# Optimization experiments

Measured on AMD Instinct MI355X. Metric: run time of the kernel, lower is better.

## Reference

```python
import jax, jax.numpy as jnp
import numpy as np

SQ, B, H, D = 2048, 1, 16, 64
HIDDEN = H * D


def setup_inputs() -> dict:
    key = jax.random.key(0)
    kq, kk, kv = jax.random.split(key, 3)
    query_layer = jax.random.normal(kq, (SQ, B, H, D), dtype=jnp.float32)
    key_layer = jax.random.normal(kk, (SQ, B, H, D), dtype=jnp.float32)
    value_layer = jax.random.normal(kv, (SQ, B, H, D), dtype=jnp.float32)
    return {"query_layer": query_layer, "key_layer": key_layer, "value_layer": value_layer}


def reference(query_layer, key_layer, value_layer):
    sq, b, h, d = query_layer.shape
    sk = key_layer.shape[0]
    norm = 1.0 / jnp.sqrt(jnp.asarray(d, dtype=query_layer.dtype))
    # scores: [b, h, sq, sk]  (materialized in the original via baddbmm)
    scores = jnp.einsum('sbhd,tbhd->bhst', query_layer, key_layer) * norm
    # causal mask (tril over [sq, sk]); masked positions -> -10000.0 as in original
    causal = jnp.tril(jnp.ones((sq, sk), dtype=bool))
    scores = jnp.where(causal[None, None], scores, jnp.asarray(-10000.0, scores.dtype))
    probs = jax.nn.softmax(scores, axis=-1)
    # context: [sq, b, h, d] -> [sq, b, hidden]
    ctx = jnp.einsum('bhst,tbhd->sbhd', probs, value_layer)
    return ctx.reshape(sq, b, h * d)
```

## Files before the change

kernel.cpp:

```cpp
#include <hip/hip_runtime.h>

typedef __bf16 bf16_t;
typedef bf16_t bf16x4 __attribute__((ext_vector_type(4)));
typedef bf16_t bf16x8 __attribute__((ext_vector_type(8)));
typedef float f32x4 __attribute__((ext_vector_type(4)));
typedef float f32x16 __attribute__((ext_vector_type(16)));

namespace {
constexpr int kNH  = 16;
constexpr int kHD  = 64;
constexpr int kHID = kNH * kHD;
constexpr int kSQ  = 2048;
constexpr int kKP  = 72;
constexpr int kOmPitch = 68;
constexpr int kSmBytes = 71680;
constexpr int kKbElems = kNH * kSQ * kHD;
}

__global__ __launch_bounds__(256)
void prep_kernel(const float* __restrict__ Kg, const float* __restrict__ Vg,
                 bf16_t* __restrict__ Kb, bf16_t* __restrict__ Vb) {
  const int bid = blockIdx.x;
  const int tid = threadIdx.x;
  if (bid < 1024) {
    const int o    = (bid * 256 + tid) * 8;
    const int head = o >> 17;
    const int t    = (o >> 6) & 2047;
    const int d0   = o & 63;
    const float4 f0 = *(const float4*)(Kg + (size_t)t * kHID + head * kHD + d0);
    const float4 f1 = *(const float4*)(Kg + (size_t)t * kHID + head * kHD + d0 + 4);
    bf16x8 hk;
    hk[0] = (bf16_t)f0.x; hk[1] = (bf16_t)f0.y; hk[2] = (bf16_t)f0.z; hk[3] = (bf16_t)f0.w;
    hk[4] = (bf16_t)f1.x; hk[5] = (bf16_t)f1.y; hk[6] = (bf16_t)f1.z; hk[7] = (bf16_t)f1.w;
    *(bf16x8*)(Kb + o) = hk;
  } else {
    const int vb   = bid - 1024;
    const int head = vb >> 6;
    const int tile = vb & 63;
    const int lane = tid >> 2;
    const int hh   = lane >> 5;
    const int m31  = lane & 31;
    const int q    = tid & 3;
    const int db   = q >> 1, tp = q & 1;
    const int tb   = tile * 32 + 4 * hh + 16 * tp;
    const int d    = m31 + 32 * db;
    const float* src = Vg + (size_t)tb * kHID + head * kHD + d;
    bf16x8 hv;
    #pragma unroll
    for (int j = 0; j < 8; ++j)
      hv[j] = (bf16_t)src[(size_t)((j & 3) + 8 * (j >> 2)) * kHID];
    *(bf16x8*)(Vb + ((size_t)(head * 64 + tile) * 64 + lane) * 32 + (db * 16 + tp * 8)) = hv;
  }
}

__global__ __launch_bounds__(512, 2)
void fattn_kernel(const float* __restrict__ Qg, const bf16_t* __restrict__ Kb,
                  const bf16_t* __restrict__ Vb, float* __restrict__ Og) {
  __shared__ __align__(16) unsigned char smraw[kSmBytes];
  bf16_t* sm = (bf16_t*)smraw;
  bf16_t* qs = sm;

  const int bid  = blockIdx.x;
  const int head = bid & (kNH - 1);
  const int ip   = bid >> 4;

  const int tid  = threadIdx.x;
  const int wave = tid >> 6;
  const int lane = tid & 63;
  const int h    = lane >> 5;
  const int m31  = lane & 31;

  const float kQScale = 0.125f * 1.44269504088896340736f;

  const bf16_t* kfb = Kb + (size_t)head * (kSQ * kHD) + (size_t)m31 * kHD + 8 * h;
  const bf16_t* vfb = Vb + ((size_t)head * 64 * 64 + lane) * 32;

  for (int halfq = 0; halfq < 2; ++halfq) {
    const int mblk = halfq ? ip : (31 - ip);
    const int m0   = mblk * 64;
    const int mtk  = 2 * mblk + 1;

    __syncthreads();
    #pragma unroll
    for (int i = 0; i < 2; ++i) {
      const int idx = tid + 512 * i;
      const int row = idx >> 4;
      const int c4  = (idx & 15) * 4;
      const float4 f = *(const float4*)(Qg + (size_t)(m0 + row) * kHID + head * kHD + c4);
      bf16x4 qv;
      qv[0] = (bf16_t)(f.x * kQScale); qv[1] = (bf16_t)(f.y * kQScale);
      qv[2] = (bf16_t)(f.z * kQScale); qv[3] = (bf16_t)(f.w * kQScale);
      *(bf16x4*)(qs + row * kKP + c4) = qv;
    }
    __syncthreads();

    bf16x8 qf00 = *(const bf16x8*)(qs + m31 * kKP +  0 + 8 * h);
    bf16x8 qf01 = *(const bf16x8*)(qs + m31 * kKP + 16 + 8 * h);
    bf16x8 qf02 = *(const bf16x8*)(qs + m31 * kKP + 32 + 8 * h);
    bf16x8 qf03 = *(const bf16x8*)(qs + m31 * kKP + 48 + 8 * h);
    bf16x8 qf10 = *(const bf16x8*)(qs + (32 + m31) * kKP +  0 + 8 * h);
    bf16x8 qf11 = *(const bf16x8*)(qs + (32 + m31) * kKP + 16 + 8 * h);
    bf16x8 qf12 = *(const bf16x8*)(qs + (32 + m31) * kKP + 32 + 8 * h);
    bf16x8 qf13 = *(const bf16x8*)(qs + (32 + m31) * kKP + 48 + 8 * h);

    f32x16 Oa00, Oa10, Oa01, Oa11;
    #pragma unroll
    for (int r = 0; r < 16; ++r) { Oa00[r] = 0.f; Oa10[r] = 0.f; Oa01[r] = 0.f; Oa11[r] = 0.f; }
    float lacc0 = 0.f, lacc1 = 0.f;

    bf16x8 k0, k1, k2, k3, v0, v1, v2, v3;
    int jt = wave;
    if (jt <= mtk) {
      const bf16_t* kp = kfb + (size_t)jt * 2048;
      k0 = *(const bf16x8*)(kp);      k1 = *(const bf16x8*)(kp + 16);
      k2 = *(const bf16x8*)(kp + 32); k3 = *(const bf16x8*)(kp + 48);
      const bf16_t* vp = vfb + (size_t)jt * 2048;
      v0 = *(const bf16x8*)(vp);      v1 = *(const bf16x8*)(vp + 8);
      v2 = *(const bf16x8*)(vp + 16); v3 = *(const bf16x8*)(vp + 24);
    }
    for (; jt <= mtk; jt += 8) {
      const int kv0  = jt * 32;
      const bool do0 = (kv0 <= m0);

      f32x16 c0, c1;
      if (do0) {
        #pragma unroll
        for (int r = 0; r < 16; ++r) c0[r] = 0.f;
        c0 = __builtin_amdgcn_mfma_f32_32x32x16_bf16(k0, qf00, c0, 0, 0, 0);
        c0 = __builtin_amdgcn_mfma_f32_32x32x16_bf16(k1, qf01, c0, 0, 0, 0);
        c0 = __builtin_amdgcn_mfma_f32_32x32x16_bf16(k2, qf02, c0, 0, 0, 0);
        c0 = __builtin_amdgcn_mfma_f32_32x32x16_bf16(k3, qf03, c0, 0, 0, 0);
      }
      #pragma unroll
      for (int r = 0; r < 16; ++r) c1[r] = 0.f;
      c1 = __builtin_amdgcn_mfma_f32_32x32x16_bf16(k0, qf10, c1, 0, 0, 0);
      c1 = __builtin_amdgcn_mfma_f32_32x32x16_bf16(k1, qf11, c1, 0, 0, 0);
      c1 = __builtin_amdgcn_mfma_f32_32x32x16_bf16(k2, qf12, c1, 0, 0, 0);
      c1 = __builtin_amdgcn_mfma_f32_32x32x16_bf16(k3, qf13, c1, 0, 0, 0);

      if (jt + 8 <= mtk) {
        const bf16_t* kp = kfb + (size_t)(jt + 8) * 2048;
        k0 = *(const bf16x8*)(kp);      k1 = *(const bf16x8*)(kp + 16);
        k2 = *(const bf16x8*)(kp + 32); k3 = *(const bf16x8*)(kp + 48);
      }

      if (do0) {
        float p[16];
        if (kv0 == m0) {
          #pragma unroll
          for (int r = 0; r < 16; ++r) {
            const int kr = (r & 3) + 8 * (r >> 2) + 4 * h;
            const float e = __builtin_amdgcn_exp2f(c0[r]);
            p[r] = (kr <= m31) ? e : 0.f;
            lacc0 += p[r];
          }
        } else {
          #pragma unroll
          for (int r = 0; r < 16; ++r) { p[r] = __builtin_amdgcn_exp2f(c0[r]); lacc0 += p[r]; }
        }
        bf16x8 pb0, pb1;
        #pragma unroll
        for (int j = 0; j < 8; ++j) { pb0[j] = (bf16_t)p[j]; pb1[j] = (bf16_t)p[8 + j]; }
        Oa00 = __builtin_amdgcn_mfma_f32_32x32x16_bf16(v0, pb0, Oa00, 0, 0, 0);
        Oa10 = __builtin_amdgcn_mfma_f32_32x32x16_bf16(v2, pb0, Oa10, 0, 0, 0);
        Oa00 = __builtin_amdgcn_mfma_f32_32x32x16_bf16(v1, pb1, Oa00, 0, 0, 0);
        Oa10 = __builtin_amdgcn_mfma_f32_32x32x16_bf16(v3, pb1, Oa10, 0, 0, 0);
      }

      {
        float p[16];
        if (kv0 == m0 + 32) {
          #pragma unroll
          for (int r = 0; r < 16; ++r) {
            const int kr = (r & 3) + 8 * (r >> 2) + 4 * h;
            const float e = __builtin_amdgcn_exp2f(c1[r]);
            p[r] = (kr <= m31) ? e : 0.f;
            lacc1 += p[r];
          }
        } else {
          #pragma unroll
          for (int r = 0; r < 16; ++r) { p[r] = __builtin_amdgcn_exp2f(c1[r]); lacc1 += p[r]; }
        }
        bf16x8 pb0, pb1;
        #pragma unroll
        for (int j = 0; j < 8; ++j) { pb0[j] = (bf16_t)p[j]; pb1[j] = (bf16_t)p[8 + j]; }
        Oa01 = __builtin_amdgcn_mfma_f32_32x32x16_bf16(v0, pb0, Oa01, 0, 0, 0);
        Oa11 = __builtin_amdgcn_mfma_f32_32x32x16_bf16(v2, pb0, Oa11, 0, 0, 0);
        Oa01 = __builtin_amdgcn_mfma_f32_32x32x16_bf16(v1, pb1, Oa01, 0, 0, 0);
        Oa11 = __builtin_amdgcn_mfma_f32_32x32x16_bf16(v3, pb1, Oa11, 0, 0, 0);
      }

      if (jt + 8 <= mtk) {
        const bf16_t* vp = vfb + (size_t)(jt + 8) * 2048;
        v0 = *(const bf16x8*)(vp);      v1 = *(const bf16x8*)(vp + 8);
        v2 = *(const bf16x8*)(vp + 16); v3 = *(const bf16x8*)(vp + 24);
      }
    }

    float* fv   = (float*)smraw;
    float* Om   = fv + wave * 32 * kOmPitch;
    float* larr = fv + 8 * 32 * kOmPitch;

    #pragma unroll
    for (int qh = 0; qh < 2; ++qh) {
      __syncthreads();
      {
        const f32x16& A0 = qh ? Oa01 : Oa00;
        const f32x16& A1 = qh ? Oa11 : Oa10;
        #pragma unroll
        for (int q = 0; q < 4; ++q) {
          f32x4 w0, w1;
          #pragma unroll
          for (int e = 0; e < 4; ++e) { w0[e] = A0[4 * q + e]; w1[e] = A1[4 * q + e]; }
          *(f32x4*)(Om + (size_t)m31 * kOmPitch + 8 * q + 4 * h)      = w0;
          *(f32x4*)(Om + (size_t)m31 * kOmPitch + 32 + 8 * q + 4 * h) = w1;
        }
        larr[wave * 64 + lane] = qh ? lacc1 : lacc0;
      }
      __syncthreads();
      {
        const int row = tid >> 4;
        const int c4  = (tid & 15) * 4;
        float l = 0.f;
        #pragma unroll
        for (int w = 0; w < 8; ++w)
          l += larr[w * 64 + row] + larr[w * 64 + 32 + row];
        const float inv = 1.f / l;
        f32x4 o;
        #pragma unroll
        for (int e = 0; e < 4; ++e) o[e] = 0.f;
        #pragma unroll
        for (int w = 0; w < 8; ++w) {
          const f32x4 a = *(const f32x4*)(fv + w * 32 * kOmPitch + (size_t)row * kOmPitch + c4);
          #pragma unroll
          for (int e = 0; e < 4; ++e) o[e] += a[e];
        }
        #pragma unroll
        for (int e = 0; e < 4; ++e) o[e] *= inv;
        *(f32x4*)(Og + (size_t)(m0 + 32 * qh + row) * kHID + head * kHD + c4) = o;
      }
    }
  }
}

extern "C" void kernel_launch(void* const* d_in, const int* in_sizes, int n_in,
                              void* d_out, int out_size, void* d_ws, size_t ws_size,
                              hipStream_t stream) {
  (void)in_sizes; (void)n_in; (void)ws_size; (void)out_size;
  const float* Q = (const float*)d_in[0];
  const float* K = (const float*)d_in[1];
  const float* V = (const float*)d_in[2];
  float* O = (float*)d_out;
  bf16_t* Kb = (bf16_t*)d_ws;
  bf16_t* Vb = Kb + kKbElems;
  hipLaunchKernelGGL(prep_kernel, dim3(2048), dim3(256), 0, stream, K, V, Kb, Vb);
  dim3 grid(256);
  dim3 block(512);
  hipLaunchKernelGGL(fattn_kernel, grid, block, 0, stream, Q, Kb, Vb, O);
}
```

Before: 93.04 us.

## Split query tile across wave halves with six KV-group waves each

Blocks grow from 8 to 12 waves. Each wave now computes a single 32-row query tile: waves are split into two halves by query rows, and within a half six waves stride over the KV tiles. This replaces the old scheme where every wave handled both 32-row query halves and wasted MFMA slots on masked tiles, and it puts more waves per CU to hide latency. MFMA sections are wrapped in s_setprio to favour matrix issue, and the epilogue reduces over six partial results per half with one fewer barrier. The cost is more shared memory per block, so fewer blocks can share a CU, and fewer registers per thread.

Result: slower. 102.0 us (+9.6%).

```diff
diff --git a/kernel.cpp b/kernel.cpp
--- a/kernel.cpp
+++ b/kernel.cpp
@@ -13,7 +13,8 @@
 constexpr int kSQ  = 2048;
 constexpr int kKP  = 72;
 constexpr int kOmPitch = 68;
-constexpr int kSmBytes = 71680;
+constexpr int kQBytes  = 9216;
+constexpr int kSmBytes = kQBytes + 12 * 32 * kOmPitch * 4 + 12 * 64 * 4;
 constexpr int kKbElems = kNH * kSQ * kHD;
 }
 
@@ -53,12 +54,11 @@
   }
 }
 
-__global__ __launch_bounds__(512, 2)
+__global__ __launch_bounds__(768, 3)
 void fattn_kernel(const float* __restrict__ Qg, const bf16_t* __restrict__ Kb,
                   const bf16_t* __restrict__ Vb, float* __restrict__ Og) {
   __shared__ __align__(16) unsigned char smraw[kSmBytes];
-  bf16_t* sm = (bf16_t*)smraw;
-  bf16_t* qs = sm;
+  bf16_t* qs = (bf16_t*)smraw;
 
   const int bid  = blockIdx.x;
   const int head = bid & (kNH - 1);
@@ -69,175 +69,148 @@
   const int lane = tid & 63;
   const int h    = lane >> 5;
   const int m31  = lane & 31;
+  const int hw   = wave / 6;
+  const int kg   = wave - 6 * hw;
 
   const float kQScale = 0.125f * 1.44269504088896340736f;
 
   const bf16_t* kfb = Kb + (size_t)head * (kSQ * kHD) + (size_t)m31 * kHD + 8 * h;
   const bf16_t* vfb = Vb + ((size_t)head * 64 * 64 + lane) * 32;
+
+  float* fv   = (float*)(smraw + kQBytes);
+  float* Om   = fv + wave * 32 * kOmPitch;
+  float* larr = fv + 12 * 32 * kOmPitch;
 
   for (int halfq = 0; halfq < 2; ++halfq) {
     const int mblk = halfq ? ip : (31 - ip);
     const int m0   = mblk * 64;
-    const int mtk  = 2 * mblk + 1;
+    const int q0   = m0 + 32 * hw;
+    const int jtmax = 2 * mblk + hw;
 
     __syncthreads();
     #pragma unroll
     for (int i = 0; i < 2; ++i) {
-      const int idx = tid + 512 * i;
-      const int row = idx >> 4;
-      const int c4  = (idx & 15) * 4;
-      const float4 f = *(const float4*)(Qg + (size_t)(m0 + row) * kHID + head * kHD + c4);
-      bf16x4 qv;
-      qv[0] = (bf16_t)(f.x * kQScale); qv[1] = (bf16_t)(f.y * kQScale);
-      qv[2] = (bf16_t)(f.z * kQScale); qv[3] = (bf16_t)(f.w * kQScale);
-      *(bf16x4*)(qs + row * kKP + c4) = qv;
+      const int idx = tid + 768 * i;
+      if (idx < 1024) {
+        const int row = idx >> 4;
+        const int c4  = (idx & 15) * 4;
+        const float4 f = *(const float4*)(Qg + (size_t)(m0 + row) * kHID + head * kHD + c4);
+        bf16x4 qv;
+        qv[0] = (bf16_t)(f.x * kQScale); qv[1] = (bf16_t)(f.y * kQScale);
+        qv[2] = (bf16_t)(f.z * kQScale); qv[3] = (bf16_t)(f.w * kQScale);
+        *(bf16x4*)(qs + row * kKP + c4) = qv;
+      }
     }
     __syncthreads();
 
-    bf16x8 qf00 = *(const bf16x8*)(qs + m31 * kKP +  0 + 8 * h);
-    bf16x8 qf01 = *(const bf16x8*)(qs + m31 * kKP + 16 + 8 * h);
-    bf16x8 qf02 = *(const bf16x8*)(qs + m31 * kKP + 32 + 8 * h);
-    bf16x8 qf03 = *(const bf16x8*)(qs + m31 * kKP + 48 + 8 * h);
-    bf16x8 qf10 = *(const bf16x8*)(qs + (32 + m31) * kKP +  0 + 8 * h);
-    bf16x8 qf11 = *(const bf16x8*)(qs + (32 + m31) * kKP + 16 + 8 * h);
-    bf16x8 qf12 = *(const bf16x8*)(qs + (32 + m31) * kKP + 32 + 8 * h);
-    bf16x8 qf13 = *(const bf16x8*)(qs + (32 + m31) * kKP + 48 + 8 * h);
-
-    f32x16 Oa00, Oa10, Oa01, Oa11;
-    #pragma unroll
-    for (int r = 0; r < 16; ++r) { Oa00[r] = 0.f; Oa10[r] = 0.f; Oa01[r] = 0.f; Oa11[r] = 0.f; }
-    float lacc0 = 0.f, lacc1 = 0.f;
+    const bf16_t* qrow = qs + (32 * hw + m31) * kKP + 8 * h;
+    bf16x8 qf0 = *(const bf16x8*)(qrow +  0);
+    bf16x8 qf1 = *(const bf16x8*)(qrow + 16);
+    bf16x8 qf2 = *(const bf16x8*)(qrow + 32);
+    bf16x8 qf3 = *(const bf16x8*)(qrow + 48);
+
+    f32x16 Oa0, Oa1;
+    #pragma unroll
+    for (int r = 0; r < 16; ++r) { Oa0[r] = 0.f; Oa1[r] = 0.f; }
+    float lacc = 0.f;
 
     bf16x8 k0, k1, k2, k3, v0, v1, v2, v3;
-    int jt = wave;
-    if (jt <= mtk) {
-      const bf16_t* kp = kfb + (size_t)jt * 2048;
+    {
+      const bf16_t* kp = kfb + (size_t)kg * 2048;
       k0 = *(const bf16x8*)(kp);      k1 = *(const bf16x8*)(kp + 16);
       k2 = *(const bf16x8*)(kp + 32); k3 = *(const bf16x8*)(kp + 48);
-      const bf16_t* vp = vfb + (size_t)jt * 2048;
+      const bf16_t* vp = vfb + (size_t)kg * 2048;
       v0 = *(const bf16x8*)(vp);      v1 = *(const bf16x8*)(vp + 8);
       v2 = *(const bf16x8*)(vp + 16); v3 = *(const bf16x8*)(vp + 24);
     }
-    for (; jt <= mtk; jt += 8) {
-      const int kv0  = jt * 32;
-      const bool do0 = (kv0 <= m0);
-
-      f32x16 c0, c1;
-      if (do0) {
-        #pragma unroll
-        for (int r = 0; r < 16; ++r) c0[r] = 0.f;
-        c0 = __builtin_amdgcn_mfma_f32_32x32x16_bf16(k0, qf00, c0, 0, 0, 0);
-        c0 = __builtin_amdgcn_mfma_f32_32x32x16_bf16(k1, qf01, c0, 0, 0, 0);
-        c0 = __builtin_amdgcn_mfma_f32_32x32x16_bf16(k2, qf02, c0, 0, 0, 0);
-        c0 = __builtin_amdgcn_mfma_f32_32x32x16_bf16(k3, qf03, c0, 0, 0, 0);
-      }
+
+    for (int jt = kg; jt <= jtmax; jt += 6) {
+      const int kv0 = jt * 32;
+      const int jn = (jt + 6 <= jtmax) ? (jt + 6) : kg;
+
+      f32x16 c;
       #pragma unroll
-      for (int r = 0; r < 16; ++r) c1[r] = 0.f;
-      c1 = __builtin_amdgcn_mfma_f32_32x32x16_bf16(k0, qf10, c1, 0, 0, 0);
-      c1 = __builtin_amdgcn_mfma_f32_32x32x16_bf16(k1, qf11, c1, 0, 0, 0);
-      c1 = __builtin_amdgcn_mfma_f32_32x32x16_bf16(k2, qf12, c1, 0, 0, 0);
-      c1 = __builtin_amdgcn_mfma_f32_32x32x16_bf16(k3, qf13, c1, 0, 0, 0);
-
-      if (jt + 8 <= mtk) {
-        const bf16_t* kp = kfb + (size_t)(jt + 8) * 2048;
+      for (int r = 0; r < 16; ++r) c[r] = 0.f;
+      __builtin_amdgcn_s_setprio(1);
+      c = __builtin_amdgcn_mfma_f32_32x32x16_bf16(k0, qf0, c, 0, 0, 0);
+      c = __builtin_amdgcn_mfma_f32_32x32x16_bf16(k1, qf1, c, 0, 0, 0);
+      c = __builtin_amdgcn_mfma_f32_32x32x16_bf16(k2, qf2, c, 0, 0, 0);
+      c = __builtin_amdgcn_mfma_f32_32x32x16_bf16(k3, qf3, c, 0, 0, 0);
+      __builtin_amdgcn_s_setprio(0);
+
+      {
+        const bf16_t* kp = kfb + (size_t)jn * 2048;
         k0 = *(const bf16x8*)(kp);      k1 = *(const bf16x8*)(kp + 16);
         k2 = *(const bf16x8*)(kp + 32); k3 = *(const bf16x8*)(kp + 48);
       }
 
-      if (do0) {
-        float p[16];
-        if (kv0 == m0) {
-          #pragma unroll
-          for (int r = 0; r < 16; ++r) {
-            const int kr = (r & 3) + 8 * (r >> 2) + 4 * h;
-            const float e = __builtin_amdgcn_exp2f(c0[r]);
-            p[r] = (kr <= m31) ? e : 0.f;
-            lacc0 += p[r];
-          }
-        } else {
-          #pragma unroll
-          for (int r = 0; r < 16; ++r) { p[r] = __builtin_amdgcn_exp2f(c0[r]); lacc0 += p[r]; }
+      float p[16];
+      if (kv0 == q0) {
+        #pragma unroll
+        for (int r = 0; r < 16; ++r) {
+          const int kr = (r & 3) + 8 * (r >> 2) + 4 * h;
+          const float e = __builtin_amdgcn_exp2f(c[r]);
+          p[r] = (kr <= m31) ? e : 0.f;
+          lacc += p[r];
         }
-        bf16x8 pb0, pb1;
-        #pragma unroll
-        for (int j = 0; j < 8; ++j) { pb0[j] = (bf16_t)p[j]; pb1[j] = (bf16_t)p[8 + j]; }
-        Oa00 = __builtin_amdgcn_mfma_f32_32x32x16_bf16(v0, pb0, Oa00, 0, 0, 0);
-        Oa10 = __builtin_amdgcn_mfma_f32_32x32x16_bf16(v2, pb0, Oa10, 0, 0, 0);
-        Oa00 = __builtin_amdgcn_mfma_f32_32x32x16_bf16(v1, pb1, Oa00, 0, 0, 0);
-        Oa10 = __builtin_amdgcn_mfma_f32_32x32x16_bf16(v3, pb1, Oa10, 0, 0, 0);
-      }
+      } else {
+        #pragma unroll
+        for (int r = 0; r < 16; ++r) { p[r] = __builtin_amdgcn_exp2f(c[r]); lacc += p[r]; }
+      }
+      bf16x8 pb0, pb1;
+      #pragma unroll
+      for (int j = 0; j < 8; ++j) { pb0[j] = (bf16_t)p[j]; pb1[j] = (bf16_t)p[8 + j]; }
+
+      __builtin_amdgcn_s_setprio(1);
+      Oa0 = __builtin_amdgcn_mfma_f32_32x32x16_bf16(v0, pb0, Oa0, 0, 0, 0);
+      Oa1 = __builtin_amdgcn_mfma_f32_32x32x16_bf16(v2, pb0, Oa1, 0, 0, 0);
+      Oa0 = __builtin_amdgcn_mfma_f32_32x32x16_bf16(v1, pb1, Oa0, 0, 0, 0);
+      Oa1 = __builtin_amdgcn_mfma_f32_32x32x16_bf16(v3, pb1, Oa1, 0, 0, 0);
+      __builtin_amdgcn_s_setprio(0);
 
       {
-        float p[16];
-        if (kv0 == m0 + 32) {
-          #pragma unroll
-          for (int r = 0; r < 16; ++r) {
-            const int kr = (r & 3) + 8 * (r >> 2) + 4 * h;
-            const float e = __builtin_amdgcn_exp2f(c1[r]);
-            p[r] = (kr <= m31) ? e : 0.f;
-            lacc1 += p[r];
-          }
-        } else {
-          #pragma unroll
-          for (int r = 0; r < 16; ++r) { p[r] = __builtin_amdgcn_exp2f(c1[r]); lacc1 += p[r]; }
-        }
-        bf16x8 pb0, pb1;
-        #pragma unroll
-        for (int j = 0; j < 8; ++j) { pb0[j] = (bf16_t)p[j]; pb1[j] = (bf16_t)p[8 + j]; }
-        Oa01 = __builtin_amdgcn_mfma_f32_32x32x16_bf16(v0, pb0, Oa01, 0, 0, 0);
-        Oa11 = __builtin_amdgcn_mfma_f32_32x32x16_bf16(v2, pb0, Oa11, 0, 0, 0);
-        Oa01 = __builtin_amdgcn_mfma_f32_32x32x16_bf16(v1, pb1, Oa01, 0, 0, 0);
-        Oa11 = __builtin_amdgcn_mfma_f32_32x32x16_bf16(v3, pb1, Oa11, 0, 0, 0);
-      }
-
-      if (jt + 8 <= mtk) {
-        const bf16_t* vp = vfb + (size_t)(jt + 8) * 2048;
+        const bf16_t* vp = vfb + (size_t)jn * 2048;
         v0 = *(const bf16x8*)(vp);      v1 = *(const bf16x8*)(vp + 8);
         v2 = *(const bf16x8*)(vp + 16); v3 = *(const bf16x8*)(vp + 24);
       }
     }
 
-    float* fv   = (float*)smraw;
-    float* Om   = fv + wave * 32 * kOmPitch;
-    float* larr = fv + 8 * 32 * kOmPitch;
-
-    #pragma unroll
-    for (int qh = 0; qh < 2; ++qh) {
-      __syncthreads();
-      {
-        const f32x16& A0 = qh ? Oa01 : Oa00;
-        const f32x16& A1 = qh ? Oa11 : Oa10;
-        #pragma unroll
-        for (int q = 0; q < 4; ++q) {
-          f32x4 w0, w1;
-          #pragma unroll
-          for (int e = 0; e < 4; ++e) { w0[e] = A0[4 * q + e]; w1[e] = A1[4 * q + e]; }
-          *(f32x4*)(Om + (size_t)m31 * kOmPitch + 8 * q + 4 * h)      = w0;
-          *(f32x4*)(Om + (size_t)m31 * kOmPitch + 32 + 8 * q + 4 * h) = w1;
-        }
-        larr[wave * 64 + lane] = qh ? lacc1 : lacc0;
-      }
-      __syncthreads();
-      {
-        const int row = tid >> 4;
-        const int c4  = (tid & 15) * 4;
+    #pragma unroll
+    for (int q = 0; q < 4; ++q) {
+      f32x4 w0, w1;
+      #pragma unroll
+      for (int e = 0; e < 4; ++e) { w0[e] = Oa0[4 * q + e]; w1[e] = Oa1[4 * q + e]; }
+      *(f32x4*)(Om + (size_t)m31 * kOmPitch + 8 * q + 4 * h)      = w0;
+      *(f32x4*)(Om + (size_t)m31 * kOmPitch + 32 + 8 * q + 4 * h) = w1;
+    }
+    larr[wave * 64 + lane] = lacc;
+    __syncthreads();
+    #pragma unroll
+    for (int i = 0; i < 2; ++i) {
+      const int idx = tid + 768 * i;
+      if (idx < 1024) {
+        const int row = idx >> 4;
+        const int c4  = (idx & 15) * 4;
+        const int r32 = row & 31;
+        const int wb  = (row >> 5) * 6;
         float l = 0.f;
         #pragma unroll
-        for (int w = 0; w < 8; ++w)
-          l += larr[w * 64 + row] + larr[w * 64 + 32 + row];
+        for (int w = 0; w < 6; ++w)
+          l += larr[(wb + w) * 64 + r32] + larr[(wb + w) * 64 + 32 + r32];
         const float inv = 1.f / l;
         f32x4 o;
         #pragma unroll
         for (int e = 0; e < 4; ++e) o[e] = 0.f;
         #pragma unroll
-        for (int w = 0; w < 8; ++w) {
-          const f32x4 a = *(const f32x4*)(fv + w * 32 * kOmPitch + (size_t)row * kOmPitch + c4);
+        for (int w = 0; w < 6; ++w) {
+          const f32x4 a = *(const f32x4*)(fv + (size_t)(wb + w) * 32 * kOmPitch
+                                             + (size_t)r32 * kOmPitch + c4);
           #pragma unroll
           for (int e = 0; e < 4; ++e) o[e] += a[e];
         }
         #pragma unroll
         for (int e = 0; e < 4; ++e) o[e] *= inv;
-        *(f32x4*)(Og + (size_t)(m0 + 32 * qh + row) * kHID + head * kHD + c4) = o;
+        *(f32x4*)(Og + (size_t)(m0 + row) * kHID + head * kHD + c4) = o;
       }
     }
   }
@@ -255,6 +228,6 @@
   bf16_t* Vb = Kb + kKbElems;
   hipLaunchKernelGGL(prep_kernel, dim3(2048), dim3(256), 0, stream, K, V, Kb, Vb);
   dim3 grid(256);
-  dim3 block(512);
+  dim3 block(768);
   hipLaunchKernelGGL(fattn_kernel, grid, block, 0, stream, Q, Kb, Vb, O);
 }
```
